# Performance work log

Measured on AMD Instinct MI355X. Metric: run time of the kernel, lower is better.

The kernel has to match this reference:

```python
import jax, jax.numpy as jnp
import numpy as np

N = 50000
E = 1600000
F_IN = 512
H1, C1 = 8, 8          # layer1: 8 heads x 8 channels, concat -> 64
C2 = 40                # layer2: 1 head, num_classes
NEG_SLOPE = 0.2


def setup_inputs() -> dict:
    key = jax.random.key(0)
    ks = jax.random.split(key, 12)
    x = jax.random.normal(ks[0], (N, F_IN), dtype=jnp.float32)
    edge_index = jax.random.randint(ks[1], (2, E), 0, N, dtype=jnp.int32)
    s1 = 1.0 / np.sqrt(F_IN)
    W1 = jax.random.uniform(ks[2], (F_IN, H1 * C1), jnp.float32, -s1, s1)
    att_src1 = jax.random.normal(ks[3], (1, H1, C1), dtype=jnp.float32) * 0.1
    att_dst1 = jax.random.normal(ks[4], (1, H1, C1), dtype=jnp.float32) * 0.1
    b1 = jnp.zeros((H1 * C1,), jnp.float32)
    s2 = 1.0 / np.sqrt(H1 * C1)
    W2 = jax.random.uniform(ks[5], (H1 * C1, C2), jnp.float32, -s2, s2)
    att_src2 = jax.random.normal(ks[6], (1, 1, C2), dtype=jnp.float32) * 0.1
    att_dst2 = jax.random.normal(ks[7], (1, 1, C2), dtype=jnp.float32) * 0.1
    b2 = jnp.zeros((C2,), jnp.float32)
    return {"x": x, "edge_index": edge_index,
            "W1": W1, "att_src1": att_src1, "att_dst1": att_dst1, "b1": b1,
            "W2": W2, "att_src2": att_src2, "att_dst2": att_dst2, "b2": b2}


def gat_conv(x, W, att_src, att_dst, bias, src, dst, heads, out_ch, concat):
    n = x.shape[0]
    h = (x @ W).reshape(n, heads, out_ch)                 # [N,H,C]
    a_src = (h * att_src).sum(-1)                          # [N,H]
    a_dst = (h * att_dst).sum(-1)                          # [N,H]
    logits = jax.nn.leaky_relu(a_src[src] + a_dst[dst], NEG_SLOPE)  # [E,H]
    # segment softmax over incoming edges per destination node
    m = jax.ops.segment_max(logits, dst, num_segments=n)   # [N,H]
    ex = jnp.exp(logits - m[dst])                          # [E,H]
    denom = jax.ops.segment_sum(ex, dst, num_segments=n)   # [N,H]
    w = ex / denom[dst]                                    # [E,H]
    out = jax.ops.segment_sum(h[src] * w[:, :, None], dst, num_segments=n)  # [N,H,C]
    if concat:
        out = out.reshape(n, heads * out_ch)
    else:
        out = out.mean(axis=1)
    return out + bias


def reference(x, edge_index, W1, att_src1, att_dst1, b1, W2, att_src2, att_dst2, b2):
    # add self loops (PyG add_self_loops=True)
    loop = jnp.arange(N, dtype=edge_index.dtype)
    src = jnp.concatenate([edge_index[0], loop])
    dst = jnp.concatenate([edge_index[1], loop])
    # dropout is identity in eval mode
    h = gat_conv(x, W1, att_src1, att_dst1, b1, src, dst, H1, C1, True)
    h = jax.nn.relu(h)
    h = gat_conv(h, W2, att_src2, att_dst2, b2, src, dst, 1, C2, False)
    return jax.nn.log_softmax(h, axis=1)
```

## Files before the change

kernel.cpp:

```cpp
#include <hip/hip_runtime.h>
#include <math.h>

#define NN 50000
#define EE 1600000
#define FIN 512
#define H1N 8
#define C2N 40
#define NEG 0.2f

#define NB 391
#define CAPG 6144
#define PA_ITEMS 8192
#define NITEMS (EE + NN)
#define PA_BLOCKS ((NITEMS + PA_ITEMS - 1) / PA_ITEMS)
#define W1T_BLOCKS 32

typedef __attribute__((ext_vector_type(8))) short bf16x8;
typedef __attribute__((ext_vector_type(4))) float f32x4;

__device__ inline short f2bf(float f) {
  unsigned int u = __float_as_uint(f);
  u += 0x7FFFu + ((u >> 16) & 1u);
  return (short)(u >> 16);
}
__device__ inline unsigned int pack2bf(float lo, float hi) {
  return (unsigned int)(unsigned short)f2bf(lo) | ((unsigned int)(unsigned short)f2bf(hi) << 16);
}
__device__ inline float bflo(unsigned int v) { return __uint_as_float(v << 16); }
__device__ inline float bfhi(unsigned int v) { return __uint_as_float(v & 0xFFFF0000u); }

__global__ __launch_bounds__(256) void passA_kernel(const int* __restrict__ ei,
    int* __restrict__ bucket_cnt, unsigned int* __restrict__ bucket_glob,
    const float* __restrict__ W1, short* __restrict__ WT) {
  int t = threadIdx.x;
  if (blockIdx.x >= PA_BLOCKS) {
    int base = (blockIdx.x - PA_BLOCKS) * 1024 + t * 4;
#pragma unroll
    for (int j = 0; j < 4; ++j) {
      int i = base + j;
      int n = i >> 9, k = i & 511;
      WT[i] = f2bf(W1[k * 64 + n]);
    }
    return;
  }
  __shared__ int hist[NB];
  __shared__ int prefix[NB];
  __shared__ int cursor[NB];
  __shared__ int gbase[NB];
  __shared__ int scA[512], scB[512];
  __shared__ unsigned int staging[PA_ITEMS];
  int i0 = blockIdx.x * PA_ITEMS;
  int count = NITEMS - i0; if (count > PA_ITEMS) count = PA_ITEMS;

  for (int b = t; b < NB; b += 256) hist[b] = 0;
  __syncthreads();
  for (int j = t; j < count; j += 256) {
    int e = i0 + j;
    int dst = (e < EE) ? ei[EE + e] : (e - EE);
    atomicAdd(&hist[dst >> 7], 1);
  }
  __syncthreads();
  scA[t]       = (t < NB) ? hist[t] : 0;
  scA[t + 256] = (t + 256 < NB) ? hist[t + 256] : 0;
  __syncthreads();
  {
    int* pa = scA; int* pb = scB;
    for (int off = 1; off < 512; off <<= 1) {
      pb[t]       = pa[t]       + (t >= off ? pa[t - off] : 0);
      pb[t + 256] = pa[t + 256] + (t + 256 >= off ? pa[t + 256 - off] : 0);
      __syncthreads();
      int* tmp = pa; pa = pb; pb = tmp;
    }
    for (int b = t; b < NB; b += 256) {
      int ex = pa[b] - hist[b];
      prefix[b] = ex;
      cursor[b] = ex;
      if (hist[b] > 0) gbase[b] = atomicAdd(&bucket_cnt[b], hist[b]);
    }
  }
  __syncthreads();
  for (int j = t; j < count; j += 256) {
    int e = i0 + j;
    int src, dst;
    if (e < EE) { src = ei[e]; dst = ei[EE + e]; }
    else        { src = e - EE; dst = src; }
    int b = dst >> 7;
    unsigned int v = (unsigned int)src | ((unsigned int)(dst & 127) << 16)
                   | ((unsigned int)b << 23);
    int lp = atomicAdd(&cursor[b], 1);
    staging[lp] = v;
  }
  __syncthreads();
  for (int j = t; j < count; j += 256) {
    unsigned int v = staging[j];
    int b = (int)(v >> 23);
    int gpos = b * CAPG + gbase[b] + (j - prefix[b]);
    bucket_glob[gpos] = v;
  }
}

__global__ __launch_bounds__(512) void scan_buckets(const int* __restrict__ bucket_cnt,
    int* __restrict__ bucket_base, int* __restrict__ row_ptr_last) {
  __shared__ int scA[512], scB[512];
  int t = threadIdx.x;
  int v = (t < NB) ? bucket_cnt[t] : 0;
  scA[t] = v;
  __syncthreads();
  int* pa = scA; int* pb = scB;
  for (int off = 1; off < 512; off <<= 1) {
    pb[t] = pa[t] + (t >= off ? pa[t - off] : 0);
    __syncthreads();
    int* tmp = pa; pa = pb; pb = tmp;
  }
  if (t < NB) bucket_base[t] = pa[t] - v;
  if (t == NB - 1) *row_ptr_last = pa[t];
}

#define CAPB 6144
__global__ __launch_bounds__(256) void passB_kernel(const unsigned int* __restrict__ bucket_glob,
    const int* __restrict__ bucket_cnt, const int* __restrict__ bucket_base,
    int* __restrict__ row_ptr, int* __restrict__ col) {
  __shared__ int hist[128], pre[128], cur[128];
  __shared__ int scA[128], scB[128];
  __shared__ int sorted[CAPB];
  int b = blockIdx.x, t = threadIdx.x;
  int cnt = bucket_cnt[b];
  int base = bucket_base[b];
  const unsigned int* in = bucket_glob + (size_t)b * CAPG;
  if (t < 128) hist[t] = 0;
  __syncthreads();
  for (int j = t; j < cnt; j += 256) {
    int dl = (int)((in[j] >> 16) & 127u);
    atomicAdd(&hist[dl], 1);
  }
  __syncthreads();
  if (t < 128) scA[t] = hist[t];
  __syncthreads();
  {
    int* pa = scA; int* pb = scB;
    for (int off = 1; off < 128; off <<= 1) {
      if (t < 128) pb[t] = pa[t] + (t >= off ? pa[t - off] : 0);
      __syncthreads();
      int* tmp = pa; pa = pb; pb = tmp;
    }
    if (t < 128) {
      int ex = pa[t] - hist[t];
      pre[t] = ex;
      cur[t] = ex;
      int d = b * 128 + t;
      if (d < NN) row_ptr[d] = base + ex;
    }
  }
  __syncthreads();
  for (int j = t; j < cnt; j += 256) {
    unsigned int v = in[j];
    int dl = (int)((v >> 16) & 127u);
    int lp = atomicAdd(&cur[dl], 1);
    sorted[lp] = (int)(v & 0xFFFFu);
  }
  __syncthreads();
  for (int j = t; j < cnt; j += 256) col[base + j] = sorted[j];
}


#define XS_STRIDE 136
#define HS_STRIDE 68
__global__ __launch_bounds__(256) void gemm1_kernel(const float* __restrict__ x,
    const short* __restrict__ WT, unsigned short* __restrict__ h1b,
    const float* __restrict__ att_src, const float* __restrict__ att_dst,
    float* __restrict__ asrc, float* __restrict__ adst) {
  __shared__ char smem[64 * XS_STRIDE * 2];
  short* xs = (short*)smem;
  float* hsf = (float*)smem;
  int t = threadIdx.x;
  int wave = t >> 6, lane = t & 63;
  int quad = lane >> 4, m = lane & 15;
  int row0 = blockIdx.x * 64;
  f32x4 acc[4] = {{0.f,0.f,0.f,0.f},{0.f,0.f,0.f,0.f},{0.f,0.f,0.f,0.f},{0.f,0.f,0.f,0.f}};
  for (int kc = 0; kc < 4; ++kc) {
    int k0 = kc * 128;
    __syncthreads();
#pragma unroll
    for (int jj = 0; jj < 8; ++jj) {
      int idx = jj * 256 + t;
      int row = idx >> 5, kq = idx & 31;
      int rr = row0 + row; if (rr >= NN) rr = NN - 1;
      float4 v = *(const float4*)(x + (size_t)rr * FIN + k0 + kq * 4);
      short4 s;
      s.x = f2bf(v.x); s.y = f2bf(v.y); s.z = f2bf(v.z); s.w = f2bf(v.w);
      *(short4*)&xs[row * XS_STRIDE + kq * 4] = s;
    }
    __syncthreads();
#pragma unroll
    for (int ks = 0; ks < 4; ++ks) {
      bf16x8 a = *(bf16x8*)&xs[(wave * 16 + m) * XS_STRIDE + ks * 32 + quad * 8];
#pragma unroll
      for (int tl = 0; tl < 4; ++tl) {
        bf16x8 b = *(const bf16x8*)(WT + (size_t)(tl * 16 + m) * 512 + k0 + ks * 32 + quad * 8);
        acc[tl] = __builtin_amdgcn_mfma_f32_16x16x32_bf16(a, b, acc[tl], 0, 0, 0);
      }
    }
  }
  __syncthreads();
  int rl0 = wave * 16 + quad * 4;
#pragma unroll
  for (int tl = 0; tl < 4; ++tl) {
#pragma unroll
    for (int r = 0; r < 4; ++r) {
      int rr = row0 + rl0 + r;
      if (rr < NN) h1b[(size_t)rr * 64 + tl * 16 + m] = (unsigned short)f2bf(acc[tl][r]);
      hsf[(rl0 + r) * HS_STRIDE + tl * 16 + m] = acc[tl][r];
    }
  }
  __syncthreads();
#pragma unroll
  for (int p = 0; p < 2; ++p) {
    int idx = p * 256 + t;
    int rl = idx >> 3, h = idx & 7;
    int rr = row0 + rl;
    if (rr < NN) {
      const float* hv = &hsf[rl * HS_STRIDE + h * 8];
      const float* as = att_src + h * 8;
      const float* ad = att_dst + h * 8;
      float s = 0.f, dd = 0.f;
#pragma unroll
      for (int c = 0; c < 8; ++c) { s = fmaf(hv[c], as[c], s); dd = fmaf(hv[c], ad[c], dd); }
      asrc[rr * 8 + h] = s;
      adst[rr * 8 + h] = dd;
    }
  }
}


__global__ __launch_bounds__(256) void l1_edge_kernel(const int* __restrict__ row_ptr,
    const int* __restrict__ col, const unsigned int* __restrict__ h1b,
    const float* __restrict__ asrc, const float* __restrict__ adst,
    const float* __restrict__ b1, const float* __restrict__ W2,
    const float* __restrict__ att_src2, const float* __restrict__ att_dst2,
    unsigned int* __restrict__ gb, float* __restrict__ asrc2, float* __restrict__ adst2) {
  __shared__ float w2s[64 * C2N];
  __shared__ float hs[4][64];
  __shared__ float gs[4][48];
  int t = threadIdx.x;
  for (int i = t; i < 64 * C2N; i += 256) w2s[i] = W2[i];
  __syncthreads();
  int d = (blockIdx.x * 256 + t) >> 6;
  int lane = t & 63;
  int wave = t >> 6;
  int half = lane >> 5, c2 = lane & 31, h = c2 >> 2;
  int start = row_ptr[d], end = row_ptr[d + 1];
  float adst_h = adst[d * 8 + h];
  float ax = 0.f, ay = 0.f, den = 0.f;
  int e = start;
  int n8 = start + ((end - start) & ~7);
  for (; e < n8; e += 8) {
    int s[4];
#pragma unroll
    for (int j = 0; j < 4; ++j) s[j] = col[e + 2 * j + half];
    float av[4];
#pragma unroll
    for (int j = 0; j < 4; ++j) av[j] = asrc[s[j] * 8 + h];
    unsigned int hv[4];
#pragma unroll
    for (int j = 0; j < 4; ++j) hv[j] = h1b[(size_t)s[j] * 32 + c2];
#pragma unroll
    for (int j = 0; j < 4; ++j) {
      float a = av[j] + adst_h;
      float logit = a > 0.f ? a : NEG * a;
      float ex = __expf(logit);
      den += ex;
      ax = fmaf(ex, bflo(hv[j]), ax);
      ay = fmaf(ex, bfhi(hv[j]), ay);
    }
  }
  for (; e + 1 < end; e += 2) {
    int s = col[e + half];
    float a = asrc[s * 8 + h] + adst_h;
    float logit = a > 0.f ? a : NEG * a;
    float ex = __expf(logit);
    unsigned int hv = h1b[(size_t)s * 32 + c2];
    den += ex;
    ax = fmaf(ex, bflo(hv), ax);
    ay = fmaf(ex, bfhi(hv), ay);
  }
  if (e < end) {
    int s = col[e];
    float a = asrc[s * 8 + h] + adst_h;
    float logit = a > 0.f ? a : NEG * a;
    float ex = (half == 0) ? __expf(logit) : 0.f;
    unsigned int hv = h1b[(size_t)s * 32 + c2];
    den += ex;
    ax = fmaf(ex, bflo(hv), ax);
    ay = fmaf(ex, bfhi(hv), ay);
  }
  ax += __shfl_xor(ax, 32);
  ay += __shfl_xor(ay, 32);
  den += __shfl_xor(den, 32);
  if (half == 0) {
    float inv = 1.f / den;
    float o0 = fmaxf(fmaf(ax, inv, 0.f) + b1[2 * c2], 0.f);
    float o1 = fmaxf(fmaf(ay, inv, 0.f) + b1[2 * c2 + 1], 0.f);
    hs[wave][2 * c2]     = o0;
    hs[wave][2 * c2 + 1] = o1;
  }
  int c = lane;
  float gacc = 0.f;
  if (c < C2N) {
#pragma unroll
    for (int k = 0; k < 64; ++k) gacc = fmaf(hs[wave][k], w2s[k * C2N + c], gacc);
  }
  float asv = (c < C2N) ? gacc * att_src2[c] : 0.f;
  float adv = (c < C2N) ? gacc * att_dst2[c] : 0.f;
#pragma unroll
  for (int off = 32; off >= 1; off >>= 1) {
    asv += __shfl_xor(asv, off);
    adv += __shfl_xor(adv, off);
  }
  if (lane == 0) { asrc2[d] = asv; adst2[d] = adv; }
  if (c < C2N) gs[wave][c] = gacc;
  if (lane < 20) gb[(size_t)d * 20 + lane] = pack2bf(gs[wave][2 * lane], gs[wave][2 * lane + 1]);
}


__global__ __launch_bounds__(256) void l2_edge_kernel(const int* __restrict__ row_ptr,
    const int* __restrict__ col, const unsigned int* __restrict__ gb,
    const float* __restrict__ asrc2, const float* __restrict__ adst2,
    const float* __restrict__ b2, float* __restrict__ out) {
  int d = (blockIdx.x * blockDim.x + threadIdx.x) >> 6;
  int lane = threadIdx.x & 63;
  if (d >= NN) return;
  int half = lane >> 5, c2 = lane & 31;
  bool act = c2 < 20;
  int cL = act ? c2 : 19;
  int start = row_ptr[d], end = row_ptr[d + 1];
  float adst_d = adst2[d];
  float ax = 0.f, ay = 0.f, den = 0.f;
  int e = start;
  int n8 = start + ((end - start) & ~7);
  for (; e < n8; e += 8) {
    int s[4];
#pragma unroll
    for (int j = 0; j < 4; ++j) s[j] = col[e + 2 * j + half];
    float av[4];
#pragma unroll
    for (int j = 0; j < 4; ++j) av[j] = asrc2[s[j]];
    unsigned int gv[4];
#pragma unroll
    for (int j = 0; j < 4; ++j) gv[j] = gb[(size_t)s[j] * 20 + cL];
#pragma unroll
    for (int j = 0; j < 4; ++j) {
      float a = av[j] + adst_d;
      float logit = a > 0.f ? a : NEG * a;
      float ex = __expf(logit);
      den += ex;
      ax = fmaf(ex, bflo(gv[j]), ax);
      ay = fmaf(ex, bfhi(gv[j]), ay);
    }
  }
  for (; e + 1 < end; e += 2) {
    int s = col[e + half];
    float a = asrc2[s] + adst_d;
    float logit = a > 0.f ? a : NEG * a;
    float ex = __expf(logit);
    unsigned int gv = gb[(size_t)s * 20 + cL];
    den += ex;
    ax = fmaf(ex, bflo(gv), ax);
    ay = fmaf(ex, bfhi(gv), ay);
  }
  if (e < end) {
    int s = col[e];
    float a = asrc2[s] + adst_d;
    float logit = a > 0.f ? a : NEG * a;
    float ex = (half == 0) ? __expf(logit) : 0.f;
    unsigned int gv = gb[(size_t)s * 20 + cL];
    den += ex;
    ax = fmaf(ex, bflo(gv), ax);
    ay = fmaf(ex, bfhi(gv), ay);
  }
  ax += __shfl_xor(ax, 32);
  ay += __shfl_xor(ay, 32);
  den += __shfl_xor(den, 32);
  float inv = 1.f / den;
  float o0 = act ? fmaf(ax, inv, 0.f) + b2[2 * c2]     : 0.f;
  float o1 = act ? fmaf(ay, inv, 0.f) + b2[2 * c2 + 1] : 0.f;
  float m = act ? fmaxf(o0, o1) : -INFINITY;
#pragma unroll
  for (int off = 16; off >= 1; off >>= 1) m = fmaxf(m, __shfl_xor(m, off));
  float es = act ? (__expf(o0 - m) + __expf(o1 - m)) : 0.f;
#pragma unroll
  for (int off = 16; off >= 1; off >>= 1) es += __shfl_xor(es, off);
  float ls = logf(es);
  if (act && half == 0)
    *(float2*)(out + (size_t)d * C2N + 2 * c2) = make_float2(o0 - m - ls, o1 - m - ls);
}


extern "C" void kernel_launch(void* const* d_in, const int* in_sizes, int n_in,
                              void* d_out, int out_size, void* d_ws, size_t ws_size,
                              hipStream_t stream) {
  const float* x        = (const float*)d_in[0];
  const int*   ei       = (const int*)d_in[1];
  const float* W1       = (const float*)d_in[2];
  const float* att_src1 = (const float*)d_in[3];
  const float* att_dst1 = (const float*)d_in[4];
  const float* b1       = (const float*)d_in[5];
  const float* W2       = (const float*)d_in[6];
  const float* att_src2 = (const float*)d_in[7];
  const float* att_dst2 = (const float*)d_in[8];
  const float* b2       = (const float*)d_in[9];
  float* out = (float*)d_out;

  char* ws = (char*)d_ws;
  size_t off = 0;
  auto alloc = [&](size_t n_elem) {
    void* p = ws + off;
    off = (off + n_elem * 4 + 255) & ~(size_t)255;
    return p;
  };
  unsigned int* h1b = (unsigned int*)alloc((size_t)NN * 32);
  unsigned int* gb  = (unsigned int*)alloc((size_t)NN * 20 + 16);
  unsigned int* bucket_glob = (unsigned int*)alloc((size_t)NB * CAPG);
  float* asrc1 = (float*)alloc((size_t)NN * 8);
  float* adst1 = (float*)alloc((size_t)NN * 8);
  float* asrc2 = (float*)alloc(NN);
  float* adst2 = (float*)alloc(NN);
  int* row_ptr = (int*)alloc(NN + 1);
  int* colv    = (int*)alloc(EE + NN);
  int* bucket_cnt  = (int*)alloc(NB);
  int* bucket_base = (int*)alloc(NB);
  short* w1t   = (short*)alloc(64 * 512 / 2);

  hipMemsetAsync(bucket_cnt, 0, NB * 4, stream);
  passA_kernel<<<PA_BLOCKS + W1T_BLOCKS, 256, 0, stream>>>(ei, bucket_cnt, bucket_glob, W1, w1t);
  scan_buckets<<<1, 512, 0, stream>>>(bucket_cnt, bucket_base, row_ptr + NN);
  passB_kernel<<<NB, 256, 0, stream>>>(bucket_glob, bucket_cnt, bucket_base, row_ptr, colv);

  gemm1_kernel<<<(NN + 63) / 64, 256, 0, stream>>>(x, w1t, (unsigned short*)h1b,
                                                   att_src1, att_dst1, asrc1, adst1);
  l1_edge_kernel<<<(NN * 64 + 255) / 256, 256, 0, stream>>>(row_ptr, colv, h1b, asrc1, adst1,
                                                            b1, W2, att_src2, att_dst2,
                                                            gb, asrc2, adst2);
  l2_edge_kernel<<<(NN * 64 + 255) / 256, 256, 0, stream>>>(row_ptr, colv, gb, asrc2, adst2, b2, out);
}
```

Measured before the change: 360.1 us.

## Remap edge-kernel lanes to 8 edges × 8 channel groups with 16-byte gathers

Both edge kernels now give each lane one head/channel group and process 8 edges per wave step, two at a time. Each gathered source row is read with a single 16-byte load instead of per-lane 4-byte loads, and the partial sums are combined by cross-lane shuffles at the end. The layer-1 kernel also processes 4 destination nodes per wave to amortize its W2 shared-memory staging, and the pass-A items per block are halved. In exchange there are more shuffle reductions, more registers per lane, and a tail of clamped-index loads at the end of each node's edge list.

```diff
diff --git a/kernel.cpp b/kernel.cpp
--- a/kernel.cpp
+++ b/kernel.cpp
@@ -10,7 +10,7 @@
 
 #define NB 391
 #define CAPG 6144
-#define PA_ITEMS 8192
+#define PA_ITEMS 4096
 #define NITEMS (EE + NN)
 #define PA_BLOCKS ((NITEMS + PA_ITEMS - 1) / PA_ITEMS)
 #define W1T_BLOCKS 32
@@ -244,81 +244,79 @@
   int t = threadIdx.x;
   for (int i = t; i < 64 * C2N; i += 256) w2s[i] = W2[i];
   __syncthreads();
-  int d = (blockIdx.x * 256 + t) >> 6;
-  int lane = t & 63;
-  int wave = t >> 6;
-  int half = lane >> 5, c2 = lane & 31, h = c2 >> 2;
-  int start = row_ptr[d], end = row_ptr[d + 1];
-  float adst_h = adst[d * 8 + h];
-  float ax = 0.f, ay = 0.f, den = 0.f;
-  int e = start;
-  int n8 = start + ((end - start) & ~7);
-  for (; e < n8; e += 8) {
-    int s[4];
-#pragma unroll
-    for (int j = 0; j < 4; ++j) s[j] = col[e + 2 * j + half];
-    float av[4];
-#pragma unroll
-    for (int j = 0; j < 4; ++j) av[j] = asrc[s[j] * 8 + h];
-    unsigned int hv[4];
-#pragma unroll
-    for (int j = 0; j < 4; ++j) hv[j] = h1b[(size_t)s[j] * 32 + c2];
-#pragma unroll
-    for (int j = 0; j < 4; ++j) {
-      float a = av[j] + adst_h;
-      float logit = a > 0.f ? a : NEG * a;
-      float ex = __expf(logit);
-      den += ex;
-      ax = fmaf(ex, bflo(hv[j]), ax);
-      ay = fmaf(ex, bfhi(hv[j]), ay);
-    }
-  }
-  for (; e + 1 < end; e += 2) {
-    int s = col[e + half];
-    float a = asrc[s * 8 + h] + adst_h;
-    float logit = a > 0.f ? a : NEG * a;
-    float ex = __expf(logit);
-    unsigned int hv = h1b[(size_t)s * 32 + c2];
-    den += ex;
-    ax = fmaf(ex, bflo(hv), ax);
-    ay = fmaf(ex, bfhi(hv), ay);
-  }
-  if (e < end) {
-    int s = col[e];
-    float a = asrc[s * 8 + h] + adst_h;
-    float logit = a > 0.f ? a : NEG * a;
-    float ex = (half == 0) ? __expf(logit) : 0.f;
-    unsigned int hv = h1b[(size_t)s * 32 + c2];
-    den += ex;
-    ax = fmaf(ex, bflo(hv), ax);
-    ay = fmaf(ex, bfhi(hv), ay);
-  }
-  ax += __shfl_xor(ax, 32);
-  ay += __shfl_xor(ay, 32);
-  den += __shfl_xor(den, 32);
-  if (half == 0) {
+  int wave = t >> 6, lane = t & 63;
+  int g = lane & 7, j = lane >> 3;
+#pragma unroll 1
+  for (int iter = 0; iter < 4; ++iter) {
+    int d = blockIdx.x * 16 + iter * 4 + wave;
+    if (d >= NN) break;
+    int start = row_ptr[d], end = row_ptr[d + 1];
+    float adst_h = adst[d * 8 + g];
+    float acc[8] = {0.f,0.f,0.f,0.f,0.f,0.f,0.f,0.f};
+    float den = 0.f;
+    for (int e = start; e < end; e += 16) {
+      int i1 = e + j, i2 = e + 8 + j;
+      int k1 = i1 < end ? i1 : end - 1;
+      int k2 = i2 < end ? i2 : end - 1;
+      int s1 = col[k1], s2 = col[k2];
+      float av1 = asrc[s1 * 8 + g];
+      float av2 = asrc[s2 * 8 + g];
+      uint4 hv1 = *(const uint4*)(h1b + (size_t)s1 * 32 + g * 4);
+      uint4 hv2 = *(const uint4*)(h1b + (size_t)s2 * 32 + g * 4);
+      float a1 = av1 + adst_h, a2 = av2 + adst_h;
+      float lg1 = fmaxf(a1, NEG * a1);
+      float lg2 = fmaxf(a2, NEG * a2);
+      float ex1 = (i1 < end) ? __expf(lg1) : 0.f;
+      float ex2 = (i2 < end) ? __expf(lg2) : 0.f;
+      den += ex1 + ex2;
+      acc[0] = fmaf(ex1, bflo(hv1.x), acc[0]); acc[0] = fmaf(ex2, bflo(hv2.x), acc[0]);
+      acc[1] = fmaf(ex1, bfhi(hv1.x), acc[1]); acc[1] = fmaf(ex2, bfhi(hv2.x), acc[1]);
+      acc[2] = fmaf(ex1, bflo(hv1.y), acc[2]); acc[2] = fmaf(ex2, bflo(hv2.y), acc[2]);
+      acc[3] = fmaf(ex1, bfhi(hv1.y), acc[3]); acc[3] = fmaf(ex2, bfhi(hv2.y), acc[3]);
+      acc[4] = fmaf(ex1, bflo(hv1.z), acc[4]); acc[4] = fmaf(ex2, bflo(hv2.z), acc[4]);
+      acc[5] = fmaf(ex1, bfhi(hv1.z), acc[5]); acc[5] = fmaf(ex2, bfhi(hv2.z), acc[5]);
+      acc[6] = fmaf(ex1, bflo(hv1.w), acc[6]); acc[6] = fmaf(ex2, bflo(hv2.w), acc[6]);
+      acc[7] = fmaf(ex1, bfhi(hv1.w), acc[7]); acc[7] = fmaf(ex2, bfhi(hv2.w), acc[7]);
+    }
+#pragma unroll
+    for (int off = 8; off <= 32; off <<= 1) {
+      den += __shfl_xor(den, off);
+#pragma unroll
+      for (int c = 0; c < 8; ++c) acc[c] += __shfl_xor(acc[c], off);
+    }
     float inv = 1.f / den;
-    float o0 = fmaxf(fmaf(ax, inv, 0.f) + b1[2 * c2], 0.f);
-    float o1 = fmaxf(fmaf(ay, inv, 0.f) + b1[2 * c2 + 1], 0.f);
-    hs[wave][2 * c2]     = o0;
-    hs[wave][2 * c2 + 1] = o1;
-  }
-  int c = lane;
-  float gacc = 0.f;
-  if (c < C2N) {
-#pragma unroll
-    for (int k = 0; k < 64; ++k) gacc = fmaf(hs[wave][k], w2s[k * C2N + c], gacc);
-  }
-  float asv = (c < C2N) ? gacc * att_src2[c] : 0.f;
-  float adv = (c < C2N) ? gacc * att_dst2[c] : 0.f;
-#pragma unroll
-  for (int off = 32; off >= 1; off >>= 1) {
-    asv += __shfl_xor(asv, off);
-    adv += __shfl_xor(adv, off);
-  }
-  if (lane == 0) { asrc2[d] = asv; adst2[d] = adv; }
-  if (c < C2N) gs[wave][c] = gacc;
-  if (lane < 20) gb[(size_t)d * 20 + lane] = pack2bf(gs[wave][2 * lane], gs[wave][2 * lane + 1]);
+    if (j == 0) {
+      float4 b1a = *(const float4*)(b1 + g * 8);
+      float4 b1b = *(const float4*)(b1 + g * 8 + 4);
+      float4 h0, h1v;
+      h0.x = fmaxf(fmaf(acc[0], inv, b1a.x), 0.f);
+      h0.y = fmaxf(fmaf(acc[1], inv, b1a.y), 0.f);
+      h0.z = fmaxf(fmaf(acc[2], inv, b1a.z), 0.f);
+      h0.w = fmaxf(fmaf(acc[3], inv, b1a.w), 0.f);
+      h1v.x = fmaxf(fmaf(acc[4], inv, b1b.x), 0.f);
+      h1v.y = fmaxf(fmaf(acc[5], inv, b1b.y), 0.f);
+      h1v.z = fmaxf(fmaf(acc[6], inv, b1b.z), 0.f);
+      h1v.w = fmaxf(fmaf(acc[7], inv, b1b.w), 0.f);
+      *(float4*)&hs[wave][g * 8]     = h0;
+      *(float4*)&hs[wave][g * 8 + 4] = h1v;
+    }
+    int c = lane;
+    float gacc = 0.f;
+    if (c < C2N) {
+#pragma unroll
+      for (int k = 0; k < 64; ++k) gacc = fmaf(hs[wave][k], w2s[k * C2N + c], gacc);
+    }
+    float asv = (c < C2N) ? gacc * att_src2[c] : 0.f;
+    float adv = (c < C2N) ? gacc * att_dst2[c] : 0.f;
+#pragma unroll
+    for (int off = 32; off >= 1; off >>= 1) {
+      asv += __shfl_xor(asv, off);
+      adv += __shfl_xor(adv, off);
+    }
+    if (lane == 0) { asrc2[d] = asv; adst2[d] = adv; }
+    if (c < C2N) gs[wave][c] = gacc;
+    if (lane < 20) gb[(size_t)d * 20 + lane] = pack2bf(gs[wave][2 * lane], gs[wave][2 * lane + 1]);
+  }
 }
 
 
@@ -326,72 +324,75 @@
     const int* __restrict__ col, const unsigned int* __restrict__ gb,
     const float* __restrict__ asrc2, const float* __restrict__ adst2,
     const float* __restrict__ b2, float* __restrict__ out) {
-  int d = (blockIdx.x * blockDim.x + threadIdx.x) >> 6;
-  int lane = threadIdx.x & 63;
+  int t = threadIdx.x;
+  int d = (blockIdx.x * 256 + t) >> 6;
   if (d >= NN) return;
-  int half = lane >> 5, c2 = lane & 31;
-  bool act = c2 < 20;
-  int cL = act ? c2 : 19;
+  int lane = t & 63;
+  int g = lane & 7, j = lane >> 3;
+  int gq = (g < 5) ? g : 4;
+  bool act = g < 5;
   int start = row_ptr[d], end = row_ptr[d + 1];
   float adst_d = adst2[d];
-  float ax = 0.f, ay = 0.f, den = 0.f;
-  int e = start;
-  int n8 = start + ((end - start) & ~7);
-  for (; e < n8; e += 8) {
-    int s[4];
-#pragma unroll
-    for (int j = 0; j < 4; ++j) s[j] = col[e + 2 * j + half];
-    float av[4];
-#pragma unroll
-    for (int j = 0; j < 4; ++j) av[j] = asrc2[s[j]];
-    unsigned int gv[4];
-#pragma unroll
-    for (int j = 0; j < 4; ++j) gv[j] = gb[(size_t)s[j] * 20 + cL];
-#pragma unroll
-    for (int j = 0; j < 4; ++j) {
-      float a = av[j] + adst_d;
-      float logit = a > 0.f ? a : NEG * a;
-      float ex = __expf(logit);
-      den += ex;
-      ax = fmaf(ex, bflo(gv[j]), ax);
-      ay = fmaf(ex, bfhi(gv[j]), ay);
-    }
-  }
-  for (; e + 1 < end; e += 2) {
-    int s = col[e + half];
-    float a = asrc2[s] + adst_d;
-    float logit = a > 0.f ? a : NEG * a;
-    float ex = __expf(logit);
-    unsigned int gv = gb[(size_t)s * 20 + cL];
-    den += ex;
-    ax = fmaf(ex, bflo(gv), ax);
-    ay = fmaf(ex, bfhi(gv), ay);
-  }
-  if (e < end) {
-    int s = col[e];
-    float a = asrc2[s] + adst_d;
-    float logit = a > 0.f ? a : NEG * a;
-    float ex = (half == 0) ? __expf(logit) : 0.f;
-    unsigned int gv = gb[(size_t)s * 20 + cL];
-    den += ex;
-    ax = fmaf(ex, bflo(gv), ax);
-    ay = fmaf(ex, bfhi(gv), ay);
-  }
-  ax += __shfl_xor(ax, 32);
-  ay += __shfl_xor(ay, 32);
-  den += __shfl_xor(den, 32);
+  float acc[8] = {0.f,0.f,0.f,0.f,0.f,0.f,0.f,0.f};
+  float den = 0.f;
+  for (int e = start; e < end; e += 16) {
+    int i1 = e + j, i2 = e + 8 + j;
+    int k1 = i1 < end ? i1 : end - 1;
+    int k2 = i2 < end ? i2 : end - 1;
+    int s1 = col[k1], s2 = col[k2];
+    float av1 = asrc2[s1], av2 = asrc2[s2];
+    uint4 g1 = *(const uint4*)(gb + (size_t)s1 * 20 + gq * 4);
+    uint4 g2 = *(const uint4*)(gb + (size_t)s2 * 20 + gq * 4);
+    float a1 = av1 + adst_d, a2 = av2 + adst_d;
+    float lg1 = fmaxf(a1, NEG * a1);
+    float lg2 = fmaxf(a2, NEG * a2);
+    float ex1 = (i1 < end) ? __expf(lg1) : 0.f;
+    float ex2 = (i2 < end) ? __expf(lg2) : 0.f;
+    den += ex1 + ex2;
+    acc[0] = fmaf(ex1, bflo(g1.x), acc[0]); acc[0] = fmaf(ex2, bflo(g2.x), acc[0]);
+    acc[1] = fmaf(ex1, bfhi(g1.x), acc[1]); acc[1] = fmaf(ex2, bfhi(g2.x), acc[1]);
+    acc[2] = fmaf(ex1, bflo(g1.y), acc[2]); acc[2] = fmaf(ex2, bflo(g2.y), acc[2]);
+    acc[3] = fmaf(ex1, bfhi(g1.y), acc[3]); acc[3] = fmaf(ex2, bfhi(g2.y), acc[3]);
+    acc[4] = fmaf(ex1, bflo(g1.z), acc[4]); acc[4] = fmaf(ex2, bflo(g2.z), acc[4]);
+    acc[5] = fmaf(ex1, bfhi(g1.z), acc[5]); acc[5] = fmaf(ex2, bfhi(g2.z), acc[5]);
+    acc[6] = fmaf(ex1, bflo(g1.w), acc[6]); acc[6] = fmaf(ex2, bflo(g2.w), acc[6]);
+    acc[7] = fmaf(ex1, bfhi(g1.w), acc[7]); acc[7] = fmaf(ex2, bfhi(g2.w), acc[7]);
+  }
+#pragma unroll
+  for (int off = 8; off <= 32; off <<= 1) {
+    den += __shfl_xor(den, off);
+#pragma unroll
+    for (int c = 0; c < 8; ++c) acc[c] += __shfl_xor(acc[c], off);
+  }
   float inv = 1.f / den;
-  float o0 = act ? fmaf(ax, inv, 0.f) + b2[2 * c2]     : 0.f;
-  float o1 = act ? fmaf(ay, inv, 0.f) + b2[2 * c2 + 1] : 0.f;
-  float m = act ? fmaxf(o0, o1) : -INFINITY;
-#pragma unroll
-  for (int off = 16; off >= 1; off >>= 1) m = fmaxf(m, __shfl_xor(m, off));
-  float es = act ? (__expf(o0 - m) + __expf(o1 - m)) : 0.f;
-#pragma unroll
-  for (int off = 16; off >= 1; off >>= 1) es += __shfl_xor(es, off);
-  float ls = logf(es);
-  if (act && half == 0)
-    *(float2*)(out + (size_t)d * C2N + 2 * c2) = make_float2(o0 - m - ls, o1 - m - ls);
+  float4 b2a = *(const float4*)(b2 + gq * 8);
+  float4 b2b = *(const float4*)(b2 + gq * 8 + 4);
+  float o[8];
+  o[0] = fmaf(acc[0], inv, b2a.x); o[1] = fmaf(acc[1], inv, b2a.y);
+  o[2] = fmaf(acc[2], inv, b2a.z); o[3] = fmaf(acc[3], inv, b2a.w);
+  o[4] = fmaf(acc[4], inv, b2b.x); o[5] = fmaf(acc[5], inv, b2b.y);
+  o[6] = fmaf(acc[6], inv, b2b.z); o[7] = fmaf(acc[7], inv, b2b.w);
+  float m = -INFINITY;
+  if (act) {
+#pragma unroll
+    for (int i = 0; i < 8; ++i) m = fmaxf(m, o[i]);
+  }
+#pragma unroll
+  for (int off = 1; off <= 4; off <<= 1) m = fmaxf(m, __shfl_xor(m, off));
+  float es = 0.f;
+  if (act) {
+#pragma unroll
+    for (int i = 0; i < 8; ++i) es += __expf(o[i] - m);
+  }
+#pragma unroll
+  for (int off = 1; off <= 4; off <<= 1) es += __shfl_xor(es, off);
+  float mls = m + logf(es);
+  if (act && j == 0) {
+    float4 r0 = make_float4(o[0] - mls, o[1] - mls, o[2] - mls, o[3] - mls);
+    float4 r1 = make_float4(o[4] - mls, o[5] - mls, o[6] - mls, o[7] - mls);
+    *(float4*)(out + (size_t)d * C2N + g * 8)     = r0;
+    *(float4*)(out + (size_t)d * C2N + g * 8 + 4) = r1;
+  }
 }
 
 
@@ -437,8 +438,8 @@
 
   gemm1_kernel<<<(NN + 63) / 64, 256, 0, stream>>>(x, w1t, (unsigned short*)h1b,
                                                    att_src1, att_dst1, asrc1, adst1);
-  l1_edge_kernel<<<(NN * 64 + 255) / 256, 256, 0, stream>>>(row_ptr, colv, h1b, asrc1, adst1,
-                                                            b1, W2, att_src2, att_dst2,
-                                                            gb, asrc2, adst2);
+  l1_edge_kernel<<<(NN + 15) / 16, 256, 0, stream>>>(row_ptr, colv, h1b, asrc1, adst1,
+                                                     b1, W2, att_src2, att_dst2,
+                                                     gb, asrc2, adst2);
   l2_edge_kernel<<<(NN * 64 + 255) / 256, 256, 0, stream>>>(row_ptr, colv, gb, asrc2, adst2, b2, out);
 }
```

Result: faster. 329.7 us (-8.4%).
